# Optimization experiments

Hardware: AMD Instinct MI355X
Metric: run time of the kernel (lower is better)

Reference implementation:

```python
import jax, jax.numpy as jnp
import numpy as np

HEADS = 16
HIDDEN = 1024
D_K = HIDDEN // HEADS


def setup_inputs() -> dict:
    key = jax.random.key(0)
    ks = jax.random.split(key, 13)
    B, S, H = 2, 2048, HIDDEN
    scale = 1.0 / np.sqrt(H)
    inp = {
        "q": jax.random.normal(ks[0], (B, S, H), jnp.float32),
        "k": jax.random.normal(ks[1], (B, S, H), jnp.float32),
        "v": jax.random.normal(ks[2], (B, S, H), jnp.float32),
        "mask": jax.random.randint(ks[3], (B, S, S), 0, 2, jnp.int32),
        # torch Linear weights: [out, in], y = x @ W.T + b
        "Wq": jax.random.normal(ks[4], (H, H), jnp.float32) * scale,
        "bq": jax.random.normal(ks[5], (H,), jnp.float32) * 0.01,
        "Wk": jax.random.normal(ks[6], (H, H), jnp.float32) * scale,
        "bk": jax.random.normal(ks[7], (H,), jnp.float32) * 0.01,
        "Wv": jax.random.normal(ks[8], (H, H), jnp.float32) * scale,
        "bv": jax.random.normal(ks[9], (H,), jnp.float32) * 0.01,
        "Wo": jax.random.normal(ks[10], (H, H), jnp.float32) * scale,
        "bo": jax.random.normal(ks[11], (H,), jnp.float32) * 0.01,
    }
    return inp


def _split_heads(x, B):
    # (B, S, H) -> (B, heads, S, d_k)
    return x.reshape(B, -1, HEADS, D_K).transpose(0, 2, 1, 3)


def reference(q, k, v, mask, Wq, bq, Wk, bk, Wv, bv, Wo, bo):
    B, S, H = q.shape
    qh = _split_heads(q @ Wq.T + bq, B)
    kh = _split_heads(k @ Wk.T + bk, B)
    vh = _split_heads(v @ Wv.T + bv, B)
    inv_sqrt_dk = 1.0 / jnp.sqrt(jnp.asarray(D_K, qh.dtype))
    logits = jnp.einsum("bhqd,bhkd->bhqk", qh, kh) * inv_sqrt_dk
    # faithful to source: masked positions get logit 1e-9 (not -inf)
    m = mask[:, None, :, :]  # broadcast over heads
    logits = jnp.where(m == 0, jnp.asarray(1e-9, logits.dtype), logits)
    scores = jax.nn.softmax(logits, axis=-1)
    o = jnp.einsum("bhqk,bhkd->bhqd", scores, vh)  # (B, heads, S, d_k)
    o = o.transpose(0, 2, 1, 3).reshape(B, S, H)
    return o @ Wo.T + bo
```

## Files before the change

### kernel.cpp

```cpp
#include <hip/hip_runtime.h>

#define SEQ   2048
#define NHEAD 16
#define DKK   64
#define HID   1024

typedef __attribute__((ext_vector_type(8))) short bf16x8;
typedef __attribute__((ext_vector_type(4))) float f32x4;

__device__ __forceinline__ unsigned short f32_bf16(float f) {
    unsigned int u = __builtin_bit_cast(unsigned int, f);
    u += 0x7fffu + ((u >> 16) & 1u);
    return (unsigned short)(u >> 16);
}

__device__ __forceinline__ unsigned int pack_bf16x2(float a, float b) {
    return (unsigned int)f32_bf16(a) | ((unsigned int)f32_bf16(b) << 16);
}

__device__ __forceinline__ void glds16(const void* g, void* l) {
    __builtin_amdgcn_global_load_lds(
        (const __attribute__((address_space(1))) unsigned int*)g,
        (__attribute__((address_space(3))) unsigned int*)l, 16, 0, 0);
}

__global__ __launch_bounds__(256)
void prep_kernel(const float* __restrict__ q, const float* __restrict__ k,
                 const float* __restrict__ v,
                 const float* __restrict__ Wq, const float* __restrict__ Wk,
                 const float* __restrict__ Wv, const float* __restrict__ Wo,
                 const int* __restrict__ mask,
                 unsigned short* __restrict__ ws, unsigned long long* __restrict__ Mb)
{
    const int bid = blockIdx.x;
    if (bid < 16384) {
        int i = bid * 256 + threadIdx.x;
        const float* src; int off;
        if (i < 1048576)      { src = q;  off = i; }
        else if (i < 2097152) { src = k;  off = i - 1048576; }
        else if (i < 3145728) { src = v;  off = i - 2097152; }
        else if (i < 3407872) { src = Wq; off = i - 3145728; }
        else if (i < 3670016) { src = Wk; off = i - 3407872; }
        else if (i < 3932160) { src = Wv; off = i - 3670016; }
        else                  { src = Wo; off = i - 3932160; }
        float4 a = ((const float4*)src)[off];
        ((uint2*)ws)[i] = make_uint2(pack_bf16x2(a.x, a.y), pack_bf16x2(a.z, a.w));
    } else {
        int idx = (bid - 16384) * 256 + threadIdx.x;
        const int* src = mask + (size_t)idx * 64;
        unsigned long long wv = 0;
        #pragma unroll
        for (int i = 0; i < 16; ++i) {
            int4 m4 = *(const int4*)(src + i * 4);
            wv |= (unsigned long long)(m4.x != 0) << (i * 4 + 0);
            wv |= (unsigned long long)(m4.y != 0) << (i * 4 + 1);
            wv |= (unsigned long long)(m4.z != 0) << (i * 4 + 2);
            wv |= (unsigned long long)(m4.w != 0) << (i * 4 + 3);
        }
        Mb[idx] = wv;
    }
}

__global__ __launch_bounds__(256, 2)
void proj_kernel(const unsigned short* __restrict__ xq, const unsigned short* __restrict__ xk,
                 const unsigned short* __restrict__ xv,
                 const unsigned short* __restrict__ Wqb, const unsigned short* __restrict__ Wkb,
                 const unsigned short* __restrict__ Wvb,
                 const float* __restrict__ bq_, const float* __restrict__ bk_,
                 const float* __restrict__ bv_,
                 unsigned short* __restrict__ Qh, unsigned short* __restrict__ Kh,
                 unsigned short* __restrict__ Vt)
{
    const int z = blockIdx.z;
    const unsigned short* X; const unsigned short* W; const float* bias;
    if (z == 0)      { X = xq; W = Wqb; bias = bq_; }
    else if (z == 1) { X = xk; W = Wkb; bias = bk_; }
    else             { X = xv; W = Wvb; bias = bv_; }

    const int m0 = blockIdx.x * 128;
    const int n0 = blockIdx.y * 128;
    const int tid  = threadIdx.x;
    const int lane = tid & 63, wid = tid >> 6;
    const int wm = (wid >> 1) * 64, wn = (wid & 1) * 64;
    const int l15 = lane & 15, quad = lane >> 4;

    __shared__ __align__(16) unsigned short As[128 * 32];
    __shared__ __align__(16) unsigned short Bs[128 * 32];

    const int r0 = tid >> 2, cg = tid & 3;
    const unsigned short* gA = X + (size_t)(m0 + r0) * HID + ((cg ^ (r0 & 3)) * 8);
    const unsigned short* gB = W + (size_t)(n0 + r0) * HID + ((cg ^ (r0 & 3)) * 8);
    unsigned short* lA0 = &As[tid * 8];
    unsigned short* lA1 = &As[(tid + 256) * 8];
    unsigned short* lB0 = &Bs[tid * 8];
    unsigned short* lB1 = &Bs[(tid + 256) * 8];

    const int cgsel = (quad ^ (l15 & 3)) * 8;

    f32x4 acc[4][4];
    #pragma unroll
    for (int i = 0; i < 4; ++i)
        #pragma unroll
        for (int j = 0; j < 4; ++j)
            acc[i][j] = f32x4{0.f, 0.f, 0.f, 0.f};

    for (int k0 = 0; k0 < HID; k0 += 32) {
        glds16(gA + k0, lA0);
        glds16(gA + (size_t)64 * HID + k0, lA1);
        glds16(gB + k0, lB0);
        glds16(gB + (size_t)64 * HID + k0, lB1);
        __syncthreads();

        bf16x8 af[4], bfr[4];
        #pragma unroll
        for (int mi = 0; mi < 4; ++mi)
            af[mi] = *(const bf16x8*)&As[(wm + mi * 16 + l15) * 32 + cgsel];
        #pragma unroll
        for (int ni = 0; ni < 4; ++ni)
            bfr[ni] = *(const bf16x8*)&Bs[(wn + ni * 16 + l15) * 32 + cgsel];
        #pragma unroll
        for (int mi = 0; mi < 4; ++mi)
            #pragma unroll
            for (int ni = 0; ni < 4; ++ni)
                acc[mi][ni] = __builtin_amdgcn_mfma_f32_16x16x32_bf16(
                    af[mi], bfr[ni], acc[mi][ni], 0, 0, 0);
        __syncthreads();
    }

    const float QSCALE = 0.18033688f;
    #pragma unroll
    for (int mi = 0; mi < 4; ++mi) {
        #pragma unroll
        for (int ni = 0; ni < 4; ++ni) {
            int n = n0 + wn + ni * 16 + l15;
            float bv = bias[n];
            int hh = n >> 6, d = n & 63;
            #pragma unroll
            for (int r = 0; r < 4; ++r) {
                int m = m0 + wm + mi * 16 + quad * 4 + r;
                int bb = m >> 11, s = m & 2047;
                float val = acc[mi][ni][r] + bv;
                if (z == 0)
                    Qh[((size_t)(bb * NHEAD + hh) * SEQ + s) * DKK + d] = f32_bf16(val * QSCALE);
                else if (z == 1)
                    Kh[((size_t)(bb * NHEAD + hh) * SEQ + s) * DKK + d] = f32_bf16(val);
                else
                    Vt[((size_t)(bb * NHEAD + hh) * DKK + d) * SEQ + s] = f32_bf16(val);
            }
        }
    }
}

__global__ __launch_bounds__(256, 4)
void attn_kernel(const unsigned short* __restrict__ Qh, const unsigned short* __restrict__ Kh,
                 const unsigned short* __restrict__ Vt,
                 const unsigned long long* __restrict__ Mb,
                 unsigned short* __restrict__ Om)
{
    const int qt = blockIdx.x;
    const int h  = blockIdx.y;
    const int b  = blockIdx.z;
    const int tid  = threadIdx.x;
    const int lane = tid & 63, w = tid >> 6;
    const int l15 = lane & 15, quad = lane >> 4;
    const int q0 = qt * 64;

    const size_t hoff = (size_t)(b * NHEAD + h) * SEQ * DKK;
    const unsigned short* Qp = Qh + hoff;
    const unsigned short* Kp = Kh + hoff;
    const unsigned short* Vp = Vt + hoff;

    __shared__ __align__(16) unsigned short Ks[2][64 * 64];
    __shared__ __align__(16) unsigned short Vs[2][64 * 64];
    __shared__ __align__(16) unsigned short Ps[4][16 * 64];

    const int sr0 = tid >> 3, ss0 = tid & 7;
    const int sr1 = sr0 + 32;
    const unsigned short* Kg0 = Kp + sr0 * DKK + ((ss0 ^ (sr0 & 7)) * 8);
    const unsigned short* Kg1 = Kp + sr1 * DKK + ((ss0 ^ (sr1 & 7)) * 8);
    const unsigned short* Vg0 = Vp + (size_t)sr0 * SEQ + ((ss0 ^ (sr0 & 7)) * 8);
    const unsigned short* Vg1 = Vp + (size_t)sr1 * SEQ + ((ss0 ^ (sr1 & 7)) * 8);

    const int swz0 = ((0 * 4 + quad) ^ (l15 & 7)) * 8;
    const int swz1 = ((1 * 4 + quad) ^ (l15 & 7)) * 8;

    glds16(Kg0, &Ks[0][tid * 8]);
    glds16(Kg1, &Ks[0][2048 + tid * 8]);
    glds16(Vg0, &Vs[0][tid * 8]);
    glds16(Vg1, &Vs[0][2048 + tid * 8]);

    bf16x8 qf[2];
    #pragma unroll
    for (int kc = 0; kc < 2; ++kc)
        qf[kc] = *(const bf16x8*)(Qp + (size_t)(q0 + w * 16 + l15) * DKK + kc * 32 + quad * 8);

    bf16x8 onesf;
    #pragma unroll
    for (int i = 0; i < 8; ++i) onesf[i] = (short)0x3F80;

    f32x4 o_acc[4];
    f32x4 l_acc = f32x4{0.f, 0.f, 0.f, 0.f};
    #pragma unroll
    for (int nd = 0; nd < 4; ++nd) o_acc[nd] = f32x4{0.f, 0.f, 0.f, 0.f};

    const unsigned long long* Mrow =
        Mb + ((size_t)b * SEQ + q0 + w * 16 + quad * 4) * (SEQ / 64);

    __syncthreads();

    for (int kt = 0; kt < SEQ / 64; ++kt) {
        const int cur = kt & 1;
        if (kt < SEQ / 64 - 1) {
            const int nb = cur ^ 1;
            glds16(Kg0 + (kt + 1) * 64 * DKK, &Ks[nb][tid * 8]);
            glds16(Kg1 + (kt + 1) * 64 * DKK, &Ks[nb][2048 + tid * 8]);
            glds16(Vg0 + (kt + 1) * 64,       &Vs[nb][tid * 8]);
            glds16(Vg1 + (kt + 1) * 64,       &Vs[nb][2048 + tid * 8]);
        }

        unsigned long long mw[4];
        #pragma unroll
        for (int r = 0; r < 4; ++r)
            mw[r] = Mrow[(size_t)r * (SEQ / 64) + kt] >> l15;

        f32x4 s[4];
        #pragma unroll
        for (int ni = 0; ni < 4; ++ni) s[ni] = f32x4{0.f, 0.f, 0.f, 0.f};
        {
            bf16x8 kb[4];
            #pragma unroll
            for (int ni = 0; ni < 4; ++ni)
                kb[ni] = *(const bf16x8*)&Ks[cur][(ni * 16 + l15) * 64 + swz0];
            #pragma unroll
            for (int ni = 0; ni < 4; ++ni)
                s[ni] = __builtin_amdgcn_mfma_f32_16x16x32_bf16(qf[0], kb[ni], s[ni], 0, 0, 0);
            #pragma unroll
            for (int ni = 0; ni < 4; ++ni)
                kb[ni] = *(const bf16x8*)&Ks[cur][(ni * 16 + l15) * 64 + swz1];
            #pragma unroll
            for (int ni = 0; ni < 4; ++ni)
                s[ni] = __builtin_amdgcn_mfma_f32_16x16x32_bf16(qf[1], kb[ni], s[ni], 0, 0, 0);
        }

        #pragma unroll
        for (int r = 0; r < 4; ++r) {
            const int prow = quad * 4 + r;
            unsigned short* pp = &Ps[w][prow * 64];
            const int rx = prow & 7;
            #pragma unroll
            for (int ni = 0; ni < 4; ++ni) {
                float e = exp2f(s[ni][r]);
                float p = ((mw[r] >> (ni * 16)) & 1) ? e : 1.0f;
                const int col = ni * 16 + l15;
                pp[(((col >> 3) ^ rx) * 8) + (col & 7)] = f32_bf16(p);
            }
        }

        {
            bf16x8 pa = *(const bf16x8*)&Ps[w][l15 * 64 + swz0];
            bf16x8 vb[4];
            #pragma unroll
            for (int nd = 0; nd < 4; ++nd)
                vb[nd] = *(const bf16x8*)&Vs[cur][(nd * 16 + l15) * 64 + swz0];
            l_acc = __builtin_amdgcn_mfma_f32_16x16x32_bf16(pa, onesf, l_acc, 0, 0, 0);
            #pragma unroll
            for (int nd = 0; nd < 4; ++nd)
                o_acc[nd] = __builtin_amdgcn_mfma_f32_16x16x32_bf16(pa, vb[nd], o_acc[nd], 0, 0, 0);

            pa = *(const bf16x8*)&Ps[w][l15 * 64 + swz1];
            #pragma unroll
            for (int nd = 0; nd < 4; ++nd)
                vb[nd] = *(const bf16x8*)&Vs[cur][(nd * 16 + l15) * 64 + swz1];
            l_acc = __builtin_amdgcn_mfma_f32_16x16x32_bf16(pa, onesf, l_acc, 0, 0, 0);
            #pragma unroll
            for (int nd = 0; nd < 4; ++nd)
                o_acc[nd] = __builtin_amdgcn_mfma_f32_16x16x32_bf16(pa, vb[nd], o_acc[nd], 0, 0, 0);
        }

        __syncthreads();
    }

    #pragma unroll
    for (int r = 0; r < 4; ++r) {
        float rinv = 1.0f / l_acc[r];
        int row = q0 + w * 16 + quad * 4 + r;
        #pragma unroll
        for (int nd = 0; nd < 4; ++nd)
            Om[((size_t)b * SEQ + row) * HID + h * DKK + nd * 16 + l15] =
                f32_bf16(o_acc[nd][r] * rinv);
    }
}

__global__ __launch_bounds__(256, 2)
void outproj_kernel(const unsigned short* __restrict__ Om, const unsigned short* __restrict__ Wob,
                    const float* __restrict__ bo_, float* __restrict__ out)
{
    const int m0 = blockIdx.x * 128;
    const int n0 = blockIdx.y * 128;
    const int tid  = threadIdx.x;
    const int lane = tid & 63, wid = tid >> 6;
    const int wm = (wid >> 1) * 64, wn = (wid & 1) * 64;
    const int l15 = lane & 15, quad = lane >> 4;

    __shared__ __align__(16) unsigned short As[128 * 32];
    __shared__ __align__(16) unsigned short Bs[128 * 32];

    const int r0 = tid >> 2, cg = tid & 3;
    const unsigned short* gA = Om + (size_t)(m0 + r0) * HID + ((cg ^ (r0 & 3)) * 8);
    const unsigned short* gB = Wob + (size_t)(n0 + r0) * HID + ((cg ^ (r0 & 3)) * 8);
    unsigned short* lA0 = &As[tid * 8];
    unsigned short* lA1 = &As[(tid + 256) * 8];
    unsigned short* lB0 = &Bs[tid * 8];
    unsigned short* lB1 = &Bs[(tid + 256) * 8];
    const int cgsel = (quad ^ (l15 & 3)) * 8;

    f32x4 acc[4][4];
    #pragma unroll
    for (int i = 0; i < 4; ++i)
        #pragma unroll
        for (int j = 0; j < 4; ++j)
            acc[i][j] = f32x4{0.f, 0.f, 0.f, 0.f};

    for (int k0 = 0; k0 < HID; k0 += 32) {
        glds16(gA + k0, lA0);
        glds16(gA + (size_t)64 * HID + k0, lA1);
        glds16(gB + k0, lB0);
        glds16(gB + (size_t)64 * HID + k0, lB1);
        __syncthreads();

        bf16x8 af[4], bfr[4];
        #pragma unroll
        for (int mi = 0; mi < 4; ++mi)
            af[mi] = *(const bf16x8*)&As[(wm + mi * 16 + l15) * 32 + cgsel];
        #pragma unroll
        for (int ni = 0; ni < 4; ++ni)
            bfr[ni] = *(const bf16x8*)&Bs[(wn + ni * 16 + l15) * 32 + cgsel];
        #pragma unroll
        for (int mi = 0; mi < 4; ++mi)
            #pragma unroll
            for (int ni = 0; ni < 4; ++ni)
                acc[mi][ni] = __builtin_amdgcn_mfma_f32_16x16x32_bf16(
                    af[mi], bfr[ni], acc[mi][ni], 0, 0, 0);
        __syncthreads();
    }

    #pragma unroll
    for (int mi = 0; mi < 4; ++mi) {
        #pragma unroll
        for (int ni = 0; ni < 4; ++ni) {
            int n = n0 + wn + ni * 16 + l15;
            float bv = bo_[n];
            #pragma unroll
            for (int r = 0; r < 4; ++r) {
                int m = m0 + wm + mi * 16 + quad * 4 + r;
                out[(size_t)m * HID + n] = acc[mi][ni][r] + bv;
            }
        }
    }
}

extern "C" void kernel_launch(void* const* d_in, const int* in_sizes, int n_in,
                              void* d_out, int out_size, void* d_ws, size_t ws_size,
                              hipStream_t stream) {
    const float* q    = (const float*)d_in[0];
    const float* k    = (const float*)d_in[1];
    const float* v    = (const float*)d_in[2];
    const int*   mask = (const int*)  d_in[3];
    const float* Wq   = (const float*)d_in[4];
    const float* bq   = (const float*)d_in[5];
    const float* Wk   = (const float*)d_in[6];
    const float* bk   = (const float*)d_in[7];
    const float* Wv   = (const float*)d_in[8];
    const float* bv   = (const float*)d_in[9];
    const float* Wo   = (const float*)d_in[10];
    const float* bo   = (const float*)d_in[11];
    float* out = (float*)d_out;

    unsigned short* ws  = (unsigned short*)d_ws;
    unsigned short* qb  = ws;
    unsigned short* kbx = ws + 4194304;
    unsigned short* vbx = ws + 8388608;
    unsigned short* Wqb = ws + 12582912;
    unsigned short* Wkb = ws + 13631488;
    unsigned short* Wvb = ws + 14680064;
    unsigned short* Wob = ws + 15728640;
    unsigned short* Qh  = ws + 16777216;
    unsigned short* Kh  = ws + 20971520;
    unsigned short* Vt  = ws + 25165824;
    unsigned short* Om  = ws;
    unsigned long long* Mb = (unsigned long long*)(ws + 29360128);

    prep_kernel<<<dim3(16896), 256, 0, stream>>>(q, k, v, Wq, Wk, Wv, Wo, mask, ws, Mb);

    proj_kernel<<<dim3(32, 8, 3), 256, 0, stream>>>(qb, kbx, vbx, Wqb, Wkb, Wvb,
                                                    bq, bk, bv, Qh, Kh, Vt);
    attn_kernel<<<dim3(32, NHEAD, 2), 256, 0, stream>>>(Qh, Kh, Vt, Mb, Om);
    outproj_kernel<<<dim3(32, 8, 1), 256, 0, stream>>>(Om, Wob, bo, out);
}
```

Baseline: 305.4 us.

## Compute transposed QK^T scores to enable vectorized P stores and single mask load

Swaps the MFMA operands so each lane holds four consecutive key columns of one query row. The probabilities can then be packed into bf16 pairs and written to LDS as one 8-byte store, replacing sixteen scalar 2-byte stores, with a new XOR swizzle for the write and read addresses. This also cuts the per-iteration mask loads from four 64-bit words to one. It further uses raw v_exp_f32 instead of exp2f and wraps the MFMA groups in s_setprio. The new swizzle must stay consistent between writer and reader, and the raw exp skips the denormal and range handling that exp2f does.

```diff
diff --git a/kernel.cpp b/kernel.cpp
--- a/kernel.cpp
+++ b/kernel.cpp
@@ -16,6 +16,12 @@
 
 __device__ __forceinline__ unsigned int pack_bf16x2(float a, float b) {
     return (unsigned int)f32_bf16(a) | ((unsigned int)f32_bf16(b) << 16);
+}
+
+__device__ __forceinline__ float fast_exp2(float x) {
+    float r;
+    asm("v_exp_f32 %0, %1" : "=v"(r) : "v"(x));
+    return r;
 }
 
 __device__ __forceinline__ void glds16(const void* g, void* l) {
@@ -184,6 +190,14 @@
     const int swz0 = ((0 * 4 + quad) ^ (l15 & 7)) * 8;
     const int swz1 = ((1 * 4 + quad) ^ (l15 & 7)) * 8;
 
+    const int xsw = l15 & 14;
+    int wadr[4];
+    #pragma unroll
+    for (int ni = 0; ni < 4; ++ni)
+        wadr[ni] = l15 * 64 + (((ni * 4 + quad) ^ xsw) * 4);
+    const int padr0 = l15 * 64 + (((quad * 2) ^ xsw) * 4);
+    const int padr1 = l15 * 64 + (((8 + quad * 2) ^ xsw) * 4);
+
     glds16(Kg0, &Ks[0][tid * 8]);
     glds16(Kg1, &Ks[0][2048 + tid * 8]);
     glds16(Vg0, &Vs[0][tid * 8]);
@@ -204,7 +218,7 @@
     for (int nd = 0; nd < 4; ++nd) o_acc[nd] = f32x4{0.f, 0.f, 0.f, 0.f};
 
     const unsigned long long* Mrow =
-        Mb + ((size_t)b * SEQ + q0 + w * 16 + quad * 4) * (SEQ / 64);
+        Mb + ((size_t)b * SEQ + q0 + w * 16 + l15) * (SEQ / 64);
 
     __syncthreads();
 
@@ -218,63 +232,64 @@
             glds16(Vg1 + (kt + 1) * 64,       &Vs[nb][2048 + tid * 8]);
         }
 
-        unsigned long long mw[4];
-        #pragma unroll
-        for (int r = 0; r < 4; ++r)
-            mw[r] = Mrow[(size_t)r * (SEQ / 64) + kt] >> l15;
-
-        f32x4 s[4];
-        #pragma unroll
-        for (int ni = 0; ni < 4; ++ni) s[ni] = f32x4{0.f, 0.f, 0.f, 0.f};
+        const unsigned long long mwq = Mrow[kt] >> (quad * 4);
+
+        f32x4 st[4];
+        #pragma unroll
+        for (int ni = 0; ni < 4; ++ni) st[ni] = f32x4{0.f, 0.f, 0.f, 0.f};
         {
             bf16x8 kb[4];
             #pragma unroll
             for (int ni = 0; ni < 4; ++ni)
                 kb[ni] = *(const bf16x8*)&Ks[cur][(ni * 16 + l15) * 64 + swz0];
-            #pragma unroll
-            for (int ni = 0; ni < 4; ++ni)
-                s[ni] = __builtin_amdgcn_mfma_f32_16x16x32_bf16(qf[0], kb[ni], s[ni], 0, 0, 0);
+            __builtin_amdgcn_s_setprio(1);
+            #pragma unroll
+            for (int ni = 0; ni < 4; ++ni)
+                st[ni] = __builtin_amdgcn_mfma_f32_16x16x32_bf16(kb[ni], qf[0], st[ni], 0, 0, 0);
+            __builtin_amdgcn_s_setprio(0);
             #pragma unroll
             for (int ni = 0; ni < 4; ++ni)
                 kb[ni] = *(const bf16x8*)&Ks[cur][(ni * 16 + l15) * 64 + swz1];
-            #pragma unroll
-            for (int ni = 0; ni < 4; ++ni)
-                s[ni] = __builtin_amdgcn_mfma_f32_16x16x32_bf16(qf[1], kb[ni], s[ni], 0, 0, 0);
-        }
-
-        #pragma unroll
-        for (int r = 0; r < 4; ++r) {
-            const int prow = quad * 4 + r;
-            unsigned short* pp = &Ps[w][prow * 64];
-            const int rx = prow & 7;
-            #pragma unroll
-            for (int ni = 0; ni < 4; ++ni) {
-                float e = exp2f(s[ni][r]);
-                float p = ((mw[r] >> (ni * 16)) & 1) ? e : 1.0f;
-                const int col = ni * 16 + l15;
-                pp[(((col >> 3) ^ rx) * 8) + (col & 7)] = f32_bf16(p);
-            }
+            __builtin_amdgcn_s_setprio(1);
+            #pragma unroll
+            for (int ni = 0; ni < 4; ++ni)
+                st[ni] = __builtin_amdgcn_mfma_f32_16x16x32_bf16(kb[ni], qf[1], st[ni], 0, 0, 0);
+            __builtin_amdgcn_s_setprio(0);
+        }
+
+        #pragma unroll
+        for (int ni = 0; ni < 4; ++ni) {
+            const unsigned int b4 = (unsigned int)(mwq >> (ni * 16)) & 0xFu;
+            float p0 = (b4 & 1u) ? fast_exp2(st[ni][0]) : 1.0f;
+            float p1 = (b4 & 2u) ? fast_exp2(st[ni][1]) : 1.0f;
+            float p2 = (b4 & 4u) ? fast_exp2(st[ni][2]) : 1.0f;
+            float p3 = (b4 & 8u) ? fast_exp2(st[ni][3]) : 1.0f;
+            *(uint2*)&Ps[w][wadr[ni]] = make_uint2(pack_bf16x2(p0, p1), pack_bf16x2(p2, p3));
         }
 
         {
-            bf16x8 pa = *(const bf16x8*)&Ps[w][l15 * 64 + swz0];
+            bf16x8 pa = *(const bf16x8*)&Ps[w][padr0];
             bf16x8 vb[4];
             #pragma unroll
             for (int nd = 0; nd < 4; ++nd)
                 vb[nd] = *(const bf16x8*)&Vs[cur][(nd * 16 + l15) * 64 + swz0];
+            __builtin_amdgcn_s_setprio(1);
             l_acc = __builtin_amdgcn_mfma_f32_16x16x32_bf16(pa, onesf, l_acc, 0, 0, 0);
             #pragma unroll
             for (int nd = 0; nd < 4; ++nd)
                 o_acc[nd] = __builtin_amdgcn_mfma_f32_16x16x32_bf16(pa, vb[nd], o_acc[nd], 0, 0, 0);
-
-            pa = *(const bf16x8*)&Ps[w][l15 * 64 + swz1];
+            __builtin_amdgcn_s_setprio(0);
+
+            pa = *(const bf16x8*)&Ps[w][padr1];
             #pragma unroll
             for (int nd = 0; nd < 4; ++nd)
                 vb[nd] = *(const bf16x8*)&Vs[cur][(nd * 16 + l15) * 64 + swz1];
+            __builtin_amdgcn_s_setprio(1);
             l_acc = __builtin_amdgcn_mfma_f32_16x16x32_bf16(pa, onesf, l_acc, 0, 0, 0);
             #pragma unroll
             for (int nd = 0; nd < 4; ++nd)
                 o_acc[nd] = __builtin_amdgcn_mfma_f32_16x16x32_bf16(pa, vb[nd], o_acc[nd], 0, 0, 0);
+            __builtin_amdgcn_s_setprio(0);
         }
 
         __syncthreads();
```

New measurement: 292.2 us. 1.05x faster.
